# Performance work log

Measured on AMD Instinct MI355X. Metric: run time of the kernel, lower is better.

Reference implementation:

```python
import jax, jax.numpy as jnp
import numpy as np

IN_F = (16, 16, 16)
OUT_F = (16, 16, 16)
RANKS = (8, 8, 8, 8, 8, 8)


def setup_inputs() -> dict:
    key = jax.random.key(0)
    ks = jax.random.split(key, 9)
    x = jax.random.normal(ks[0], (4096, int(np.prod(IN_F))), dtype=jnp.float32)
    # core ~ U[0,1)*0.1 as in torch.rand(ranks)*0.1
    core = jax.random.uniform(ks[1], RANKS, dtype=jnp.float32) * 0.1
    # factor matrices: 3 out-side (out_f[i], r[i]) then 3 in-side (in_f[i], r[i+3])
    shapes = [(OUT_F[i], RANKS[i]) for i in range(3)] + [(IN_F[i], RANKS[i + 3]) for i in range(3)]
    f0, f1, f2, f3, f4, f5 = [
        jax.random.normal(ks[2 + i], shapes[i], dtype=jnp.float32) * 0.1 for i in range(6)
    ]
    bias = jnp.zeros((int(np.prod(OUT_F)),), dtype=jnp.float32)
    return {"x": x, "core": core, "f0": f0, "f1": f1, "f2": f2,
            "f3": f3, "f4": f4, "f5": f5, "bias": bias}


def reference(x, core, f0, f1, f2, f3, f4, f5, bias):
    # x: [N, prod(IN_F)] -> [N, i1, i2, i3]
    xr = x.reshape(-1, *IN_F)
    # Reconstruct full dense weight from Tucker factors (faithful to original)
    # core: [r0..r5]; f0..f2 out-side (out_dim, r); f3..f5 in-side (in_dim, r)
    W = jnp.einsum('ijklmn,ai,bj,ck,dl,em,fn->abcdef', core, f0, f1, f2, f3, f4, f5)
    # Contract input with in-side modes: [N, o1, o2, o3]
    res = jnp.einsum('abcdef,ndef->nabc', W, xr)
    y = res.reshape(-1, int(np.prod(OUT_F)))
    return y + bias
```

## Files before the change

kernel.cpp:

```cpp
#include <hip/hip_runtime.h>

#define THREADS 256

typedef __attribute__((ext_vector_type(8))) short bf16x8;
typedef __attribute__((ext_vector_type(4))) float f32x4;

__device__ inline unsigned short f2bf(float f) {
    union { float f; unsigned int u; } v; v.f = f;
    unsigned int r = v.u + 0x7fffu + ((v.u >> 16) & 1u);
    return (unsigned short)(r >> 16);
}

__global__ __launch_bounds__(THREADS) void k_in_contract(
    const float* __restrict__ x,
    const float* __restrict__ f3, const float* __restrict__ f4,
    const float* __restrict__ f5,
    unsigned short* __restrict__ u3b, int N)
{
    const int n = blockIdx.x;
    const int t = threadIdx.x;

    __shared__ float fs[256];
    __shared__ float u1s[256 * 9];
    __shared__ float u2s[128 * 9];

    if (t < 128) { fs[t] = f3[t]; fs[128 + t] = f4[t]; }

    float xv[16];
    {
        const float4* xr = (const float4*)(x + (size_t)n * 4096 + t * 16);
        float4 a0 = xr[0], a1 = xr[1], a2 = xr[2], a3 = xr[3];
        xv[0]=a0.x; xv[1]=a0.y; xv[2]=a0.z; xv[3]=a0.w;
        xv[4]=a1.x; xv[5]=a1.y; xv[6]=a1.z; xv[7]=a1.w;
        xv[8]=a2.x; xv[9]=a2.y; xv[10]=a2.z; xv[11]=a2.w;
        xv[12]=a3.x; xv[13]=a3.y; xv[14]=a3.z; xv[15]=a3.w;
    }

    float acc8[8];
    #pragma unroll
    for (int q = 0; q < 8; ++q) acc8[q] = 0.f;
    #pragma unroll
    for (int f = 0; f < 16; ++f) {
        const float xf = xv[f];
        #pragma unroll
        for (int n6 = 0; n6 < 8; ++n6)
            acc8[n6] = fmaf(xf, f5[f*8 + n6], acc8[n6]);
    }
    __syncthreads();
    #pragma unroll
    for (int n6 = 0; n6 < 8; ++n6) u1s[t*9 + n6] = acc8[n6];
    __syncthreads();

    {
        const int d = t >> 4, m = (t >> 1) & 7, h = t & 1;
        float fr[16];
        #pragma unroll
        for (int e = 0; e < 16; ++e) fr[e] = fs[128 + e*8 + m];
        float a4[4] = {0.f, 0.f, 0.f, 0.f};
        #pragma unroll
        for (int e = 0; e < 16; ++e) {
            const int base = (d*16 + e)*9 + h*4;
            #pragma unroll
            for (int q = 0; q < 4; ++q)
                a4[q] = fmaf(u1s[base + q], fr[e], a4[q]);
        }
        #pragma unroll
        for (int q = 0; q < 4; ++q) u2s[(d*8 + m)*9 + h*4 + q] = a4[q];
    }
    __syncthreads();

    {
        const int l = t >> 5, m = (t >> 2) & 7, h = t & 3;
        float fr[16];
        #pragma unroll
        for (int d = 0; d < 16; ++d) fr[d] = fs[d*8 + l];
        float a2[2] = {0.f, 0.f};
        #pragma unroll
        for (int d = 0; d < 16; ++d) {
            const int base = (d*8 + m)*9 + h*2;
            a2[0] = fmaf(u2s[base],     fr[d], a2[0]);
            a2[1] = fmaf(u2s[base + 1], fr[d], a2[1]);
        }
        unsigned int pk = (unsigned int)f2bf(a2[0]) |
                          ((unsigned int)f2bf(a2[1]) << 16);
        ((unsigned int*)u3b)[(size_t)n * 256 + t] = pk;
    }
}

__global__ __launch_bounds__(THREADS) void k_convert_core(
    const float* __restrict__ core, unsigned short* __restrict__ coreb)
{
    const int i = blockIdx.x * THREADS + threadIdx.x;
    float4 c = ((const float4*)core)[i];
    ushort4 o;
    o.x = f2bf(c.x); o.y = f2bf(c.y); o.z = f2bf(c.z); o.w = f2bf(c.w);
    ((ushort4*)coreb)[i] = o;
}

__global__ __launch_bounds__(THREADS, 8) void k_core_gemm2(
    const unsigned short* __restrict__ u3b,
    const unsigned short* __restrict__ coreb,
    float* __restrict__ v, int N)
{
    const int t    = threadIdx.x;
    const int lane = t & 63;
    const int wave = t >> 6;
    const int m0 = blockIdx.x * 16;
    const int p0 = blockIdx.y * 64 + wave * 16;
    const int lr = lane & 15;
    const int lq = lane >> 4;

    const unsigned short* ap = u3b   + (size_t)(m0 + lr) * 512 + lq * 8;
    const unsigned short* bp = coreb + (size_t)(p0 + lr) * 512 + lq * 8;

    f32x4 acc = {0.f, 0.f, 0.f, 0.f};
    #pragma unroll
    for (int kt = 0; kt < 16; ++kt) {
        bf16x8 a = *(const bf16x8*)(ap + kt * 32);
        bf16x8 b = *(const bf16x8*)(bp + kt * 32);
        acc = __builtin_amdgcn_mfma_f32_16x16x32_bf16(a, b, acc, 0, 0, 0);
    }

    const int row = m0 + lq * 4;
    const int col = p0 + lr;
    #pragma unroll
    for (int r = 0; r < 4; ++r)
        v[(size_t)(row + r) * 512 + col] = acc[r];
}

#define EXW 4

__global__ __launch_bounds__(THREADS, 4) void k_out_expand2(
    const float* __restrict__ v,
    const float* __restrict__ f0, const float* __restrict__ f1,
    const float* __restrict__ f2, const float* __restrict__ bias,
    float* __restrict__ y, int N)
{
    const int t    = threadIdx.x;
    const int wave = t >> 6;
    const int lane = t & 63;
    const int row  = blockIdx.x * EXW + wave;
    const int a = lane >> 2;
    const int s = lane & 3;

    __shared__ float vs[EXW][512];
    __shared__ float w1s[EXW][16 * 68];

    {
        const float4* vp = (const float4*)(v + (size_t)row * 512);
        float4 v0 = vp[lane * 2];
        float4 v1 = vp[lane * 2 + 1];
        float4* d = (float4*)&vs[wave][lane * 8];
        d[0] = v0; d[1] = v1;
    }
    asm volatile("s_waitcnt lgkmcnt(0)" ::: "memory");
    __builtin_amdgcn_sched_barrier(0);

    {
        float fr[8];
        #pragma unroll
        for (int i = 0; i < 8; ++i) fr[i] = f0[a * 8 + i];
        #pragma unroll
        for (int cmb = 0; cmb < 4; ++cmb) {
            const int idx = cmb * 4 + s;
            float ax = 0.f, ay = 0.f, az = 0.f, aw = 0.f;
            #pragma unroll
            for (int i = 0; i < 8; ++i) {
                float4 vv = *(const float4*)&vs[wave][i * 64 + idx * 4];
                const float fi = fr[i];
                ax = fmaf(vv.x, fi, ax); ay = fmaf(vv.y, fi, ay);
                az = fmaf(vv.z, fi, az); aw = fmaf(vv.w, fi, aw);
            }
            *(float4*)&w1s[wave][a * 68 + idx * 4] = make_float4(ax, ay, az, aw);
        }
    }
    asm volatile("s_waitcnt lgkmcnt(0)" ::: "memory");
    __builtin_amdgcn_sched_barrier(0);

    {
        float w1r[64];
        #pragma unroll
        for (int m = 0; m < 16; ++m) {
            float4 q = *(const float4*)&w1s[wave][a * 68 + m * 4];
            w1r[m*4+0] = q.x; w1r[m*4+1] = q.y;
            w1r[m*4+2] = q.z; w1r[m*4+3] = q.w;
        }
        #pragma unroll
        for (int s2 = 0; s2 < 4; ++s2) {
            const int b = s2 * 4 + s;
            float fb[8];
            #pragma unroll
            for (int j = 0; j < 8; ++j) fb[j] = f1[b * 8 + j];

            float w2[8] = {0.f,0.f,0.f,0.f,0.f,0.f,0.f,0.f};
            #pragma unroll
            for (int j = 0; j < 8; ++j) {
                const float fj = fb[j];
                #pragma unroll
                for (int k = 0; k < 8; ++k)
                    w2[k] = fmaf(w1r[j * 8 + k], fj, w2[k]);
            }

            const int ob = a * 256 + b * 16;
            const float4* bp4 = (const float4*)(bias + ob);
            float4* op = (float4*)(y + (size_t)row * 4096 + ob);
            #pragma unroll
            for (int cq = 0; cq < 4; ++cq) {
                float4 bb = bp4[cq];
                float r0 = bb.x, r1 = bb.y, r2 = bb.z, r3 = bb.w;
                #pragma unroll
                for (int k = 0; k < 8; ++k) {
                    r0 = fmaf(w2[k], f2[(cq*4 + 0) * 8 + k], r0);
                    r1 = fmaf(w2[k], f2[(cq*4 + 1) * 8 + k], r1);
                    r2 = fmaf(w2[k], f2[(cq*4 + 2) * 8 + k], r2);
                    r3 = fmaf(w2[k], f2[(cq*4 + 3) * 8 + k], r3);
                }
                op[cq] = make_float4(r0, r1, r2, r3);
            }
        }
    }
}

extern "C" void kernel_launch(void* const* d_in, const int* in_sizes, int n_in,
                              void* d_out, int out_size, void* d_ws, size_t ws_size,
                              hipStream_t stream)
{
    const float* x    = (const float*)d_in[0];
    const float* core = (const float*)d_in[1];
    const float* f0   = (const float*)d_in[2];
    const float* f1   = (const float*)d_in[3];
    const float* f2   = (const float*)d_in[4];
    const float* f3   = (const float*)d_in[5];
    const float* f4   = (const float*)d_in[6];
    const float* f5   = (const float*)d_in[7];
    const float* bias = (const float*)d_in[8];
    float* y = (float*)d_out;

    const int N = in_sizes[0] / 4096;

    unsigned short* u3b   = (unsigned short*)d_ws;
    unsigned short* coreb = u3b + (size_t)N * 512;
    float*          v     = (float*)(coreb + 512 * 512);

    k_in_contract<<<N, THREADS, 0, stream>>>(x, f3, f4, f5, u3b, N);
    k_convert_core<<<256, THREADS, 0, stream>>>(core, coreb);
    dim3 gb(N / 16, 512 / 64);
    k_core_gemm2<<<gb, THREADS, 0, stream>>>(u3b, coreb, v, N);
    k_out_expand2<<<N / EXW, THREADS, 0, stream>>>(v, f0, f1, f2, bias, y, N);
}
```

Measured before the change: 178.0 us.

## Swap GEMM block tiling to share core tile; restructure mode-1 expansion loop

The core GEMM now gives each block four waves covering different rows of u3 that share one 16-column slice of the core, instead of one u3 row tile shared across four core column tiles. This changes which operand is reused within a block and the grid shape. The output-expansion kernel now computes all four f1 contractions in a single pass over w1, reading w1 from shared memory once per j rather than staging 64 values in registers. That cuts register pressure, but the four accumulator sets add registers of their own.

```diff
diff --git a/kernel.cpp b/kernel.cpp
--- a/kernel.cpp
+++ b/kernel.cpp
@@ -97,7 +97,7 @@
     ((ushort4*)coreb)[i] = o;
 }
 
-__global__ __launch_bounds__(THREADS, 8) void k_core_gemm2(
+__global__ __launch_bounds__(THREADS, 8) void k_core_gemm3(
     const unsigned short* __restrict__ u3b,
     const unsigned short* __restrict__ coreb,
     float* __restrict__ v, int N)
@@ -105,8 +105,8 @@
     const int t    = threadIdx.x;
     const int lane = t & 63;
     const int wave = t >> 6;
-    const int m0 = blockIdx.x * 16;
-    const int p0 = blockIdx.y * 64 + wave * 16;
+    const int m0 = blockIdx.x * 64 + wave * 16;
+    const int p0 = blockIdx.y * 16;
     const int lr = lane & 15;
     const int lq = lane >> 4;
 
@@ -130,7 +130,7 @@
 
 #define EXW 4
 
-__global__ __launch_bounds__(THREADS, 4) void k_out_expand2(
+__global__ __launch_bounds__(THREADS, 4) void k_out_expand3(
     const float* __restrict__ v,
     const float* __restrict__ f0, const float* __restrict__ f1,
     const float* __restrict__ f2, const float* __restrict__ bias,
@@ -178,32 +178,44 @@
     __builtin_amdgcn_sched_barrier(0);
 
     {
-        float w1r[64];
-        #pragma unroll
-        for (int m = 0; m < 16; ++m) {
-            float4 q = *(const float4*)&w1s[wave][a * 68 + m * 4];
-            w1r[m*4+0] = q.x; w1r[m*4+1] = q.y;
-            w1r[m*4+2] = q.z; w1r[m*4+3] = q.w;
-        }
-        #pragma unroll
-        for (int s2 = 0; s2 < 4; ++s2) {
-            const int b = s2 * 4 + s;
-            float fb[8];
-            #pragma unroll
-            for (int j = 0; j < 8; ++j) fb[j] = f1[b * 8 + j];
-
-            float w2[8] = {0.f,0.f,0.f,0.f,0.f,0.f,0.f,0.f};
-            #pragma unroll
-            for (int j = 0; j < 8; ++j) {
-                const float fj = fb[j];
-                #pragma unroll
-                for (int k = 0; k < 8; ++k)
-                    w2[k] = fmaf(w1r[j * 8 + k], fj, w2[k]);
+        float w2_0[8] = {0.f,0.f,0.f,0.f,0.f,0.f,0.f,0.f};
+        float w2_1[8] = {0.f,0.f,0.f,0.f,0.f,0.f,0.f,0.f};
+        float w2_2[8] = {0.f,0.f,0.f,0.f,0.f,0.f,0.f,0.f};
+        float w2_3[8] = {0.f,0.f,0.f,0.f,0.f,0.f,0.f,0.f};
+
+        float fb0[8], fb1[8], fb2[8], fb3[8];
+        #pragma unroll
+        for (int j = 0; j < 8; ++j) {
+            fb0[j] = f1[(0*4 + s) * 8 + j];
+            fb1[j] = f1[(1*4 + s) * 8 + j];
+            fb2[j] = f1[(2*4 + s) * 8 + j];
+            fb3[j] = f1[(3*4 + s) * 8 + j];
+        }
+
+        #pragma unroll
+        for (int j = 0; j < 8; ++j) {
+            float4 wlo = *(const float4*)&w1s[wave][a * 68 + j * 8];
+            float4 whi = *(const float4*)&w1s[wave][a * 68 + j * 8 + 4];
+            const float wj[8] = {wlo.x, wlo.y, wlo.z, wlo.w,
+                                 whi.x, whi.y, whi.z, whi.w};
+            #pragma unroll
+            for (int k = 0; k < 8; ++k) {
+                w2_0[k] = fmaf(wj[k], fb0[j], w2_0[k]);
+                w2_1[k] = fmaf(wj[k], fb1[j], w2_1[k]);
+                w2_2[k] = fmaf(wj[k], fb2[j], w2_2[k]);
+                w2_3[k] = fmaf(wj[k], fb3[j], w2_3[k]);
             }
-
+        }
+
+        float* yrow = y + (size_t)row * 4096;
+        #pragma unroll
+        for (int bq = 0; bq < 4; ++bq) {
+            const float* w2 = (bq == 0) ? w2_0 : (bq == 1) ? w2_1
+                             : (bq == 2) ? w2_2 : w2_3;
+            const int b = bq * 4 + s;
             const int ob = a * 256 + b * 16;
             const float4* bp4 = (const float4*)(bias + ob);
-            float4* op = (float4*)(y + (size_t)row * 4096 + ob);
+            float4* op = (float4*)(yrow + ob);
             #pragma unroll
             for (int cq = 0; cq < 4; ++cq) {
                 float4 bb = bp4[cq];
@@ -244,7 +256,7 @@
 
     k_in_contract<<<N, THREADS, 0, stream>>>(x, f3, f4, f5, u3b, N);
     k_convert_core<<<256, THREADS, 0, stream>>>(core, coreb);
-    dim3 gb(N / 16, 512 / 64);
-    k_core_gemm2<<<gb, THREADS, 0, stream>>>(u3b, coreb, v, N);
-    k_out_expand2<<<N / EXW, THREADS, 0, stream>>>(v, f0, f1, f2, bias, y, N);
-}
+    dim3 gb(N / 64, 512 / 16);
+    k_core_gemm3<<<gb, THREADS, 0, stream>>>(u3b, coreb, v, N);
+    k_out_expand3<<<N / EXW, THREADS, 0, stream>>>(v, f0, f1, f2, bias, y, N);
+}
```

Measured after the change: 184.0 us. 1.03x slower.
